# Kernel optimization log

Hardware: AMD Instinct MI355X
Metric: run time of the kernel (lower is better)

## Reference

```python
import jax, jax.numpy as jnp
import numpy as np

N_QUBITS = 4
Q_DEPTH = 6
Q_DELTA = 0.01
BATCH = 65536


def _apply_ry(state, theta, q):
    """Apply RY(theta) on qubit q. state: [B,2,2,2,2]; theta: [B] (per-sample) or scalar.
    RY = [[cos(t/2), -sin(t/2)], [sin(t/2), cos(t/2)]] (PennyLane convention, real)."""
    c = jnp.cos(theta * 0.5)
    s = jnp.sin(theta * 0.5)
    s0 = jnp.take(state, 0, axis=q + 1)  # [B,2,2,2]
    s1 = jnp.take(state, 1, axis=q + 1)
    if jnp.ndim(theta) == 1:  # per-sample angle -> broadcast over remaining qubit axes
        c = c[:, None, None, None]
        s = s[:, None, None, None]
    new0 = c * s0 - s * s1
    new1 = s * s0 + c * s1
    return jnp.stack([new0, new1], axis=q + 1)


def _cnot(state, ctrl, tgt):
    """CNOT with control `ctrl`, target `tgt` on state [B,2,2,2,2]."""
    s0 = jnp.take(state, 0, axis=ctrl + 1)
    s1 = jnp.take(state, 1, axis=ctrl + 1)
    # target axis index inside the reduced (rank-4) array
    t_ax = tgt + 1 if tgt < ctrl else tgt
    s1 = jnp.flip(s1, axis=t_ax)
    return jnp.stack([s0, s1], axis=ctrl + 1)


def quantum_circuit(q_in, q_params):
    """Batched 4-qubit variational circuit. q_in: [B,4], q_params: [24].
    Circuit is real-valued (H, RY, CNOT on |0...0>), so state is float."""
    B = q_in.shape[0]
    # H layer on |0000> -> uniform amplitude 1/4 over all 16 basis states
    state = jnp.full((B, 2, 2, 2, 2), 0.25, dtype=q_in.dtype)
    for q in range(N_QUBITS):
        state = _apply_ry(state, q_in[:, q], q)
    qw = q_params.reshape(Q_DEPTH, N_QUBITS)
    for k in range(Q_DEPTH):
        # entangling layer: CNOT(0,1), CNOT(2,3), then CNOT(1,2)
        state = _cnot(state, 0, 1)
        state = _cnot(state, 2, 3)
        state = _cnot(state, 1, 2)
        for q in range(N_QUBITS):
            state = _apply_ry(state, qw[k, q], q)
    probs = state * state  # [B,2,2,2,2]
    zs = []
    for q in range(N_QUBITS):
        other = tuple(a for a in (1, 2, 3, 4) if a != q + 1)
        m = probs.sum(axis=other)  # [B,2]
        zs.append(m[:, 0] - m[:, 1])  # <Z_q> = P(0) - P(1)
    return jnp.stack(zs, axis=1)  # [B,4]


def setup_inputs() -> dict:
    key = jax.random.key(0)
    k1, k2, k3, k4 = jax.random.split(key, 4)
    return {
        "input_features": jax.random.normal(k1, (BATCH, 512), dtype=jnp.float32),
        "W_pre": jax.random.normal(k2, (N_QUBITS, 512), dtype=jnp.float32) * (1.0 / np.sqrt(512.0)),
        "b_pre": jnp.zeros((N_QUBITS,), dtype=jnp.float32),
        "q_params": Q_DELTA * jax.random.normal(k3, (Q_DEPTH * N_QUBITS,), dtype=jnp.float32),
        "W_post": jax.random.normal(k4, (200, N_QUBITS), dtype=jnp.float32) * 0.5,
        "b_post": jnp.zeros((200,), dtype=jnp.float32),
    }


def reference(input_features, W_pre, b_pre, q_params, W_post, b_post):
    pre_out = input_features @ W_pre.T + b_pre          # [B,4]
    q_in = jnp.tanh(pre_out) * (np.pi / 2.0)            # scale to (-pi/2, pi/2)
    q_out = quantum_circuit(q_in, q_params)             # [B,4]
    return q_out @ W_post.T + b_post                    # [B,200]
```

## Files before the change

kernel.cpp:

```cpp
#include <hip/hip_runtime.h>


#define BLOCK 256
#define WS 16
#define SPB 64

__device__ __forceinline__ float wred64(float v) {
  v += __shfl_xor(v, 32, 64);
  v += __shfl_xor(v, 16, 64);
  v += __shfl_xor(v, 8, 64);
  v += __shfl_xor(v, 4, 64);
  v += __shfl_xor(v, 2, 64);
  v += __shfl_xor(v, 1, 64);
  return v;
}

template<int Q>
__device__ __forceinline__ void apply_ry(float (&st)[16], float c, float s) {
  constexpr int pos = 3 - Q;
  #pragma unroll
  for (int i = 0; i < 16; ++i) {
    if (((i >> pos) & 1) == 0) {
      const int j = i | (1 << pos);
      const float a = st[i], b = st[j];
      st[i] = c * a - s * b;
      st[j] = s * a + c * b;
    }
  }
}

template<int C, int T>
__device__ __forceinline__ void cnot(float (&st)[16]) {
  constexpr int pc = 3 - C, pt = 3 - T;
  #pragma unroll
  for (int i = 0; i < 16; ++i) {
    if ((((i >> pc) & 1) == 1) && (((i >> pt) & 1) == 0)) {
      const int j = i | (1 << pt);
      const float t = st[i]; st[i] = st[j]; st[j] = t;
    }
  }
}

__global__ __launch_bounds__(BLOCK, 4) void dqnet_kernel(
    const float* __restrict__ in, const float* __restrict__ Wpre,
    const float* __restrict__ bpre, const float* __restrict__ qp,
    const float* __restrict__ Wpost, const float* __restrict__ bpost,
    float* __restrict__ out) {
  __shared__ float s_wpost[200 * 4];
  __shared__ float s_bpost[200];
  __shared__ float s_c[24];
  __shared__ float s_sn[24];
  __shared__ float s_qout[SPB * 4];

  const int tid = threadIdx.x;
  const int lane = tid & 63;
  const int wave = tid >> 6;

  if (tid < 200) {
    ((float4*)s_wpost)[tid] = ((const float4*)Wpost)[tid];
    s_bpost[tid] = bpost[tid];
  } else if (tid < 224) {
    const int k = tid - 200;
    const float a = qp[k] * 0.5f;
    s_c[k] = __cosf(a);
    s_sn[k] = __sinf(a);
  }

  float4 wa[4], wb[4];
  #pragma unroll
  for (int q = 0; q < 4; ++q) {
    wa[q] = *(const float4*)(Wpre + q * 512 + lane * 4);
    wb[q] = *(const float4*)(Wpre + q * 512 + 256 + lane * 4);
  }

  const int tile = blockIdx.x * SPB + wave * WS;
  const float* rb = in + (size_t)tile * 512 + lane * 4;

  float r0 = 0.f, r1 = 0.f, r2 = 0.f, r3 = 0.f;
  float4 xa = *(const float4*)rb;
  float4 xb = *(const float4*)(rb + 256);
  #pragma unroll 4
  for (int s2 = 0; s2 < WS; ++s2) {
    float4 na = xa, nb = xb;
    if (s2 + 1 < WS) {
      na = *(const float4*)(rb + (size_t)(s2 + 1) * 512);
      nb = *(const float4*)(rb + (size_t)(s2 + 1) * 512 + 256);
    }
    float p0 = xa.x*wa[0].x + xa.y*wa[0].y + xa.z*wa[0].z + xa.w*wa[0].w
             + xb.x*wb[0].x + xb.y*wb[0].y + xb.z*wb[0].z + xb.w*wb[0].w;
    float p1 = xa.x*wa[1].x + xa.y*wa[1].y + xa.z*wa[1].z + xa.w*wa[1].w
             + xb.x*wb[1].x + xb.y*wb[1].y + xb.z*wb[1].z + xb.w*wb[1].w;
    float p2 = xa.x*wa[2].x + xa.y*wa[2].y + xa.z*wa[2].z + xa.w*wa[2].w
             + xb.x*wb[2].x + xb.y*wb[2].y + xb.z*wb[2].z + xb.w*wb[2].w;
    float p3 = xa.x*wa[3].x + xa.y*wa[3].y + xa.z*wa[3].z + xa.w*wa[3].w
             + xb.x*wb[3].x + xb.y*wb[3].y + xb.z*wb[3].z + xb.w*wb[3].w;
    p0 = wred64(p0); p1 = wred64(p1); p2 = wred64(p2); p3 = wred64(p3);
    if (lane == s2) { r0 = p0; r1 = p1; r2 = p2; r3 = p3; }
    xa = na; xb = nb;
  }

  __syncthreads();

  if (lane < WS) {
    constexpr float PI_4 = 0.7853981633974483f;
    float st[16];
    #pragma unroll
    for (int i = 0; i < 16; ++i) st[i] = 0.25f;

    const float pre0 = r0 + bpre[0], pre1 = r1 + bpre[1];
    const float pre2 = r2 + bpre[2], pre3 = r3 + bpre[3];
    float sv, cv;
    __sincosf(tanhf(pre0) * PI_4, &sv, &cv); apply_ry<0>(st, cv, sv);
    __sincosf(tanhf(pre1) * PI_4, &sv, &cv); apply_ry<1>(st, cv, sv);
    __sincosf(tanhf(pre2) * PI_4, &sv, &cv); apply_ry<2>(st, cv, sv);
    __sincosf(tanhf(pre3) * PI_4, &sv, &cv); apply_ry<3>(st, cv, sv);

    #pragma unroll
    for (int k = 0; k < 6; ++k) {
      cnot<0,1>(st); cnot<2,3>(st); cnot<1,2>(st);
      apply_ry<0>(st, s_c[k*4+0], s_sn[k*4+0]);
      apply_ry<1>(st, s_c[k*4+1], s_sn[k*4+1]);
      apply_ry<2>(st, s_c[k*4+2], s_sn[k*4+2]);
      apply_ry<3>(st, s_c[k*4+3], s_sn[k*4+3]);
    }

    float p[16];
    #pragma unroll
    for (int i = 0; i < 16; ++i) p[i] = st[i] * st[i];
    float z0 = 0.f, z1 = 0.f, z2 = 0.f, z3 = 0.f;
    #pragma unroll
    for (int i = 0; i < 16; ++i) {
      z0 += ((i >> 3) & 1) ? -p[i] : p[i];
      z1 += ((i >> 2) & 1) ? -p[i] : p[i];
      z2 += ((i >> 1) & 1) ? -p[i] : p[i];
      z3 += ((i     ) & 1) ? -p[i] : p[i];
    }
    const int sl = wave * WS + lane;
    *(float4*)&s_qout[sl * 4] = make_float4(z0, z1, z2, z3);
  }
  __syncthreads();

  float* ob = out + (size_t)blockIdx.x * SPB * 200;
  #pragma unroll 2
  for (int idx = tid; idx < SPB * 200; idx += BLOCK) {
    const int sloc = idx / 200;
    const int j = idx - sloc * 200;
    const float4 qo = *(const float4*)&s_qout[sloc * 4];
    const float4 w  = *(const float4*)&s_wpost[j * 4];
    ob[idx] = s_bpost[j] + qo.x * w.x + qo.y * w.y + qo.z * w.z + qo.w * w.w;
  }
}

extern "C" void kernel_launch(void* const* d_in, const int* in_sizes, int n_in,
                              void* d_out, int out_size, void* d_ws, size_t ws_size,
                              hipStream_t stream) {
  const float* in    = (const float*)d_in[0];
  const float* Wpre  = (const float*)d_in[1];
  const float* bpre  = (const float*)d_in[2];
  const float* qp    = (const float*)d_in[3];
  const float* Wpost = (const float*)d_in[4];
  const float* bpost = (const float*)d_in[5];
  float* out = (float*)d_out;

  const int B = in_sizes[0] / 512;
  const int nblk = B / SPB;
  dqnet_kernel<<<nblk, BLOCK, 0, stream>>>(in, Wpre, bpre, qp, Wpost, bpost, out);
}
```

Before: 222.4 us.

## Use reduce-scatter shuffles, nontemporal loads, and vectorized nontemporal output stores

Replaces the per-sample full butterfly reductions (6 shuffles for each of 4 outputs per sample) with a reduce-scatter tree that spreads the 64 partial sums across lanes. This cuts the total shuffle count, and a final gather collects each sample's four dot products. Input rows are read with nontemporal loads. The output projection now writes float4 vectors with nontemporal stores instead of scalar stores. The fully unrolled loop and the 16-entry partial array add register pressure.

```diff
diff --git a/kernel.cpp b/kernel.cpp
--- a/kernel.cpp
+++ b/kernel.cpp
@@ -5,14 +5,16 @@
 #define WS 16
 #define SPB 64
 
-__device__ __forceinline__ float wred64(float v) {
-  v += __shfl_xor(v, 32, 64);
-  v += __shfl_xor(v, 16, 64);
-  v += __shfl_xor(v, 8, 64);
-  v += __shfl_xor(v, 4, 64);
-  v += __shfl_xor(v, 2, 64);
-  v += __shfl_xor(v, 1, 64);
-  return v;
+typedef float f4 __attribute__((ext_vector_type(4)));
+
+__device__ __forceinline__ f4 ntload4(const float* p) {
+  return __builtin_nontemporal_load((const f4*)p);
+}
+
+__device__ __forceinline__ float rs_step(float v0, float v1, bool hi, int m) {
+  const float sd = hi ? v0 : v1;
+  const float kp = hi ? v1 : v0;
+  return kp + __shfl_xor(sd, m, 64);
 }
 
 template<int Q>
@@ -48,16 +50,15 @@
     float* __restrict__ out) {
   __shared__ float s_wpost[200 * 4];
   __shared__ float s_bpost[200];
-  __shared__ float s_c[24];
-  __shared__ float s_sn[24];
-  __shared__ float s_qout[SPB * 4];
+  __shared__ float s_c[24], s_sn[24];
+  __shared__ f4 s_qout[SPB];
 
   const int tid = threadIdx.x;
   const int lane = tid & 63;
   const int wave = tid >> 6;
 
   if (tid < 200) {
-    ((float4*)s_wpost)[tid] = ((const float4*)Wpost)[tid];
+    ((f4*)s_wpost)[tid] = ((const f4*)Wpost)[tid];
     s_bpost[tid] = bpost[tid];
   } else if (tid < 224) {
     const int k = tid - 200;
@@ -66,25 +67,28 @@
     s_sn[k] = __sinf(a);
   }
 
-  float4 wa[4], wb[4];
+  f4 wa[4], wb[4];
   #pragma unroll
   for (int q = 0; q < 4; ++q) {
-    wa[q] = *(const float4*)(Wpre + q * 512 + lane * 4);
-    wb[q] = *(const float4*)(Wpre + q * 512 + 256 + lane * 4);
+    wa[q] = *(const f4*)(Wpre + q * 512 + lane * 4);
+    wb[q] = *(const f4*)(Wpre + q * 512 + 256 + lane * 4);
   }
 
   const int tile = blockIdx.x * SPB + wave * WS;
   const float* rb = in + (size_t)tile * 512 + lane * 4;
 
-  float r0 = 0.f, r1 = 0.f, r2 = 0.f, r3 = 0.f;
-  float4 xa = *(const float4*)rb;
-  float4 xb = *(const float4*)(rb + 256);
-  #pragma unroll 4
-  for (int s2 = 0; s2 < WS; ++s2) {
-    float4 na = xa, nb = xb;
-    if (s2 + 1 < WS) {
-      na = *(const float4*)(rb + (size_t)(s2 + 1) * 512);
-      nb = *(const float4*)(rb + (size_t)(s2 + 1) * 512 + 256);
+  const bool b1 = (lane & 1) != 0;
+  const bool b2 = (lane & 2) != 0;
+
+  float part[WS];
+  f4 xa = ntload4(rb);
+  f4 xb = ntload4(rb + 256);
+  #pragma unroll
+  for (int s = 0; s < WS; ++s) {
+    f4 na = xa, nb = xb;
+    if (s + 1 < WS) {
+      na = ntload4(rb + (size_t)(s + 1) * 512);
+      nb = ntload4(rb + (size_t)(s + 1) * 512 + 256);
     }
     float p0 = xa.x*wa[0].x + xa.y*wa[0].y + xa.z*wa[0].z + xa.w*wa[0].w
              + xb.x*wb[0].x + xb.y*wb[0].y + xb.z*wb[0].z + xb.w*wb[0].w;
@@ -94,10 +98,29 @@
              + xb.x*wb[2].x + xb.y*wb[2].y + xb.z*wb[2].z + xb.w*wb[2].w;
     float p3 = xa.x*wa[3].x + xa.y*wa[3].y + xa.z*wa[3].z + xa.w*wa[3].w
              + xb.x*wb[3].x + xb.y*wb[3].y + xb.z*wb[3].z + xb.w*wb[3].w;
-    p0 = wred64(p0); p1 = wred64(p1); p2 = wred64(p2); p3 = wred64(p3);
-    if (lane == s2) { r0 = p0; r1 = p1; r2 = p2; r3 = p3; }
+    const float a01 = rs_step(p0, p1, b1, 1);
+    const float a23 = rs_step(p2, p3, b1, 1);
+    part[s] = rs_step(a01, a23, b2, 2);
     xa = na; xb = nb;
   }
+
+  const bool b4  = (lane & 4)  != 0;
+  const bool b8  = (lane & 8)  != 0;
+  const bool b16 = (lane & 16) != 0;
+  const bool b32 = (lane & 32) != 0;
+  float a8[8], a4[4], a2[2];
+  #pragma unroll
+  for (int u = 0; u < 8; ++u) a8[u] = rs_step(part[2*u], part[2*u+1], b4, 4);
+  #pragma unroll
+  for (int u = 0; u < 4; ++u) a4[u] = rs_step(a8[2*u], a8[2*u+1], b8, 8);
+  #pragma unroll
+  for (int u = 0; u < 2; ++u) a2[u] = rs_step(a4[2*u], a4[2*u+1], b16, 16);
+  const float r = rs_step(a2[0], a2[1], b32, 32);
+
+  const float g0 = __shfl(r, (lane << 2) | 0, 64);
+  const float g1 = __shfl(r, (lane << 2) | 1, 64);
+  const float g2 = __shfl(r, (lane << 2) | 2, 64);
+  const float g3 = __shfl(r, (lane << 2) | 3, 64);
 
   __syncthreads();
 
@@ -107,13 +130,11 @@
     #pragma unroll
     for (int i = 0; i < 16; ++i) st[i] = 0.25f;
 
-    const float pre0 = r0 + bpre[0], pre1 = r1 + bpre[1];
-    const float pre2 = r2 + bpre[2], pre3 = r3 + bpre[3];
     float sv, cv;
-    __sincosf(tanhf(pre0) * PI_4, &sv, &cv); apply_ry<0>(st, cv, sv);
-    __sincosf(tanhf(pre1) * PI_4, &sv, &cv); apply_ry<1>(st, cv, sv);
-    __sincosf(tanhf(pre2) * PI_4, &sv, &cv); apply_ry<2>(st, cv, sv);
-    __sincosf(tanhf(pre3) * PI_4, &sv, &cv); apply_ry<3>(st, cv, sv);
+    __sincosf(tanhf(g0 + bpre[0]) * PI_4, &sv, &cv); apply_ry<0>(st, cv, sv);
+    __sincosf(tanhf(g1 + bpre[1]) * PI_4, &sv, &cv); apply_ry<1>(st, cv, sv);
+    __sincosf(tanhf(g2 + bpre[2]) * PI_4, &sv, &cv); apply_ry<2>(st, cv, sv);
+    __sincosf(tanhf(g3 + bpre[3]) * PI_4, &sv, &cv); apply_ry<3>(st, cv, sv);
 
     #pragma unroll
     for (int k = 0; k < 6; ++k) {
@@ -135,19 +156,28 @@
       z2 += ((i >> 1) & 1) ? -p[i] : p[i];
       z3 += ((i     ) & 1) ? -p[i] : p[i];
     }
-    const int sl = wave * WS + lane;
-    *(float4*)&s_qout[sl * 4] = make_float4(z0, z1, z2, z3);
+    f4 z; z.x = z0; z.y = z1; z.z = z2; z.w = z3;
+    s_qout[wave * WS + lane] = z;
   }
   __syncthreads();
 
-  float* ob = out + (size_t)blockIdx.x * SPB * 200;
-  #pragma unroll 2
-  for (int idx = tid; idx < SPB * 200; idx += BLOCK) {
-    const int sloc = idx / 200;
-    const int j = idx - sloc * 200;
-    const float4 qo = *(const float4*)&s_qout[sloc * 4];
-    const float4 w  = *(const float4*)&s_wpost[j * 4];
-    ob[idx] = s_bpost[j] + qo.x * w.x + qo.y * w.y + qo.z * w.z + qo.w * w.w;
+  float* ob = out + (size_t)blockIdx.x * (SPB * 200);
+  #pragma unroll
+  for (int i = 0; i < 13; ++i) {
+    const int idx4 = tid + i * BLOCK;
+    if (idx4 < 3200) {
+      const int sloc = idx4 / 50;
+      const int j4 = idx4 - sloc * 50;
+      const f4 qo = s_qout[sloc];
+      const f4* wrow = (const f4*)&s_wpost[j4 * 16];
+      const float* br = &s_bpost[j4 * 4];
+      f4 o;
+      o.x = br[0] + wrow[0].x*qo.x + wrow[0].y*qo.y + wrow[0].z*qo.z + wrow[0].w*qo.w;
+      o.y = br[1] + wrow[1].x*qo.x + wrow[1].y*qo.y + wrow[1].z*qo.z + wrow[1].w*qo.w;
+      o.z = br[2] + wrow[2].x*qo.x + wrow[2].y*qo.y + wrow[2].z*qo.z + wrow[2].w*qo.w;
+      o.w = br[3] + wrow[3].x*qo.x + wrow[3].y*qo.y + wrow[3].z*qo.z + wrow[3].w*qo.w;
+      __builtin_nontemporal_store(o, (f4*)(ob + (size_t)idx4 * 4));
+    }
   }
 }
 
```

Measured after the change: 205.4 us. -7.7%, faster.
